# Kernel tuning notes

Measured on AMD Instinct MI355X. Metric: run time of the kernel, lower is better.

## Reference

```python
import jax, jax.numpy as jnp
import numpy as np

BINS = 64
LAMBDA_AFFINE = 1.0
LAMBDA_SIM = 1.0
EPS = 1e-10

B, C, D, H, W = 2, 1, 192, 224, 192


def setup_inputs() -> dict:
    key = jax.random.key(0)
    k1, k2, k3, k4 = jax.random.split(key, 4)
    return {
        "predicted_affine": jax.random.normal(k1, (B, 12), dtype=jnp.float32),
        "true_affine": jax.random.normal(k2, (B, 12), dtype=jnp.float32),
        "fixed": jax.random.uniform(k3, (B, C, D, H, W), dtype=jnp.float32),
        "warped": jax.random.uniform(k4, (B, C, D, H, W), dtype=jnp.float32),
    }


def _bin_indices(x_flat):
    # x_flat: (B, N) -> int32 bin indices in [0, BINS-1]
    xmin = x_flat.min(axis=1, keepdims=True)
    xmax = x_flat.max(axis=1, keepdims=True)
    norm = (x_flat - xmin) / (xmax - xmin + EPS) * (BINS - 1)
    return jnp.clip(norm.astype(jnp.int32), 0, BINS - 1)


def mutual_information(fixed, warped):
    # take first channel, flatten per sample
    f = fixed[:, 0].reshape(fixed.shape[0], -1)   # (B, N)
    w = warped[:, 0].reshape(warped.shape[0], -1)  # (B, N)
    b = f.shape[0]
    fi = _bin_indices(f)
    wi = _bin_indices(w)
    # joint histogram per batch via one fused scatter-add (segment_sum)
    batch_off = (jnp.arange(b, dtype=jnp.int32) * (BINS * BINS))[:, None]
    flat_idx = (batch_off + fi * BINS + wi).reshape(-1)
    counts = jax.ops.segment_sum(
        jnp.ones(flat_idx.shape, dtype=jnp.float32), flat_idx,
        num_segments=b * BINS * BINS)
    joint = counts.reshape(b, BINS, BINS)
    joint = joint / (joint.sum(axis=(1, 2), keepdims=True) + EPS)
    p_f = joint.sum(axis=2)  # (B, BINS)
    p_w = joint.sum(axis=1)  # (B, BINS)
    h_f = -jnp.sum(p_f * jnp.log(p_f + EPS), axis=1)
    h_w = -jnp.sum(p_w * jnp.log(p_w + EPS), axis=1)
    h_j = -jnp.sum(joint * jnp.log(joint + EPS), axis=(1, 2))
    mi = h_f + h_w - h_j
    nmi = 2.0 * mi / (h_f + h_w + EPS)  # normalized=True
    return -nmi.mean()


def reference(predicted_affine, true_affine, fixed, warped):
    affine_loss = jnp.mean((predicted_affine - true_affine) ** 2)
    similarity_loss = mutual_information(fixed, warped)
    total_loss = LAMBDA_AFFINE * affine_loss + LAMBDA_SIM * similarity_loss
    return total_loss
```

## Files before the change

kernel.cpp:

```cpp
#include <hip/hip_runtime.h>
#include <cfloat>
#include <math.h>

#define BINS 64
#define NELEM (192*224*192)
#define NB 2
#define HIST_OFF 16

__device__ __forceinline__ unsigned fkey(float f){
    unsigned u = __float_as_uint(f);
    return (u & 0x80000000u) ? ~u : (u | 0x80000000u);
}
__device__ __forceinline__ float funkey(unsigned k){
    unsigned u = (k & 0x80000000u) ? (k ^ 0x80000000u) : ~k;
    return __uint_as_float(u);
}

__global__ void k_init(unsigned* ws){
    int i = blockIdx.x * 256 + threadIdx.x;
    if (i < 16) ws[i] = ((i & 1) == 0) ? 0xFFFFFFFFu : 0u;
    if (i < NB * BINS * BINS) ws[HIST_OFF + i] = 0u;
}

__global__ void k_minmax(const float* __restrict__ F, const float* __restrict__ W,
                         unsigned* ws){
    const int b = blockIdx.y;
    const float4* F4 = (const float4*)(F + (size_t)b * NELEM);
    const float4* W4 = (const float4*)(W + (size_t)b * NELEM);
    const int n4 = NELEM / 4;
    float fmn = FLT_MAX, fmx = -FLT_MAX, wmn = FLT_MAX, wmx = -FLT_MAX;
    for (int i = blockIdx.x * blockDim.x + threadIdx.x; i < n4;
         i += gridDim.x * blockDim.x){
        float4 a = F4[i], c = W4[i];
        fmn = fminf(fmn, fminf(fminf(a.x, a.y), fminf(a.z, a.w)));
        fmx = fmaxf(fmx, fmaxf(fmaxf(a.x, a.y), fmaxf(a.z, a.w)));
        wmn = fminf(wmn, fminf(fminf(c.x, c.y), fminf(c.z, c.w)));
        wmx = fmaxf(wmx, fmaxf(fmaxf(c.x, c.y), fmaxf(c.z, c.w)));
    }
    for (int off = 32; off; off >>= 1){
        fmn = fminf(fmn, __shfl_down(fmn, off));
        fmx = fmaxf(fmx, __shfl_down(fmx, off));
        wmn = fminf(wmn, __shfl_down(wmn, off));
        wmx = fmaxf(wmx, __shfl_down(wmx, off));
    }
    __shared__ float s[4][4];
    int wave = threadIdx.x >> 6;
    if ((threadIdx.x & 63) == 0){
        s[wave][0] = fmn; s[wave][1] = fmx; s[wave][2] = wmn; s[wave][3] = wmx;
    }
    __syncthreads();
    if (threadIdx.x == 0){
        float a0 = s[0][0], a1 = s[0][1], a2 = s[0][2], a3 = s[0][3];
        for (int wv = 1; wv < 4; ++wv){
            a0 = fminf(a0, s[wv][0]); a1 = fmaxf(a1, s[wv][1]);
            a2 = fminf(a2, s[wv][2]); a3 = fmaxf(a3, s[wv][3]);
        }
        atomicMin(&ws[b*4+0], fkey(a0));
        atomicMax(&ws[b*4+1], fkey(a1));
        atomicMin(&ws[b*4+2], fkey(a2));
        atomicMax(&ws[b*4+3], fkey(a3));
    }
}

__global__ void k_hist(const float* __restrict__ F, const float* __restrict__ W,
                       unsigned* ws){
    const int b = blockIdx.y;
    __shared__ unsigned h[BINS * BINS];
    for (int i = threadIdx.x; i < BINS * BINS; i += blockDim.x) h[i] = 0u;
    __syncthreads();
    const float fmn = funkey(ws[b*4+0]);
    const float fmx = funkey(ws[b*4+1]);
    const float wmn = funkey(ws[b*4+2]);
    const float wmx = funkey(ws[b*4+3]);
    const float fden = fmx - fmn + 1e-10f;
    const float wden = wmx - wmn + 1e-10f;
    const float4* F4 = (const float4*)(F + (size_t)b * NELEM);
    const float4* W4 = (const float4*)(W + (size_t)b * NELEM);
    const int n4 = NELEM / 4;
    for (int i = blockIdx.x * blockDim.x + threadIdx.x; i < n4;
         i += gridDim.x * blockDim.x){
        float4 a = F4[i], c = W4[i];
        float fa[4] = {a.x, a.y, a.z, a.w};
        float wa[4] = {c.x, c.y, c.z, c.w};
        #pragma unroll
        for (int k = 0; k < 4; ++k){
            int fi = (int)((fa[k] - fmn) / fden * 63.0f);
            int wi = (int)((wa[k] - wmn) / wden * 63.0f);
            fi = min(max(fi, 0), 63);
            wi = min(max(wi, 0), 63);
            atomicAdd(&h[fi * BINS + wi], 1u);
        }
    }
    __syncthreads();
    unsigned* gh = ws + HIST_OFF + b * BINS * BINS;
    for (int i = threadIdx.x; i < BINS * BINS; i += blockDim.x){
        unsigned v = h[i];
        if (v) atomicAdd(&gh[i], v);
    }
}

__device__ double block_sum256(double v, double* sred){
    int t = threadIdx.x;
    sred[t] = v; __syncthreads();
    for (int off = 128; off; off >>= 1){
        if (t < off) sred[t] += sred[t + off];
        __syncthreads();
    }
    double r = sred[0]; __syncthreads();
    return r;
}

__global__ void k_final(const float* __restrict__ pa, const float* __restrict__ ta,
                        const unsigned* __restrict__ ws, float* __restrict__ out){
    __shared__ double sred[256];
    const unsigned* hist = ws + HIST_OFF;
    const double invN = 1.0 / (double)NELEM;
    double loss_sim = 0.0;
    for (int b = 0; b < NB; ++b){
        const unsigned* H = hist + b * BINS * BINS;
        double hj_p = 0.0;
        for (int i = threadIdx.x; i < BINS * BINS; i += 256){
            double p = (double)H[i] * invN;
            hj_p += p * log(p + 1e-10);
        }
        double hj = -block_sum256(hj_p, sred);
        double hf_p = 0.0, hw_p = 0.0;
        if (threadIdx.x < BINS){
            int r = threadIdx.x;
            double pf = 0.0, pw = 0.0;
            for (int j = 0; j < BINS; ++j){
                pf += (double)H[r * BINS + j];
                pw += (double)H[j * BINS + r];
            }
            pf *= invN; pw *= invN;
            hf_p = pf * log(pf + 1e-10);
            hw_p = pw * log(pw + 1e-10);
        }
        double hf = -block_sum256(hf_p, sred);
        double hw = -block_sum256(hw_p, sred);
        double mi  = hf + hw - hj;
        double nmi = 2.0 * mi / (hf + hw + 1e-10);
        loss_sim += -nmi;
    }
    loss_sim /= (double)NB;
    if (threadIdx.x == 0){
        double a = 0.0;
        for (int i = 0; i < 24; ++i){
            double d = (double)pa[i] - (double)ta[i];
            a += d * d;
        }
        a /= 24.0;
        out[0] = (float)(a + loss_sim);
    }
}

extern "C" void kernel_launch(void* const* d_in, const int* in_sizes, int n_in,
                              void* d_out, int out_size, void* d_ws, size_t ws_size,
                              hipStream_t stream) {
    const float* pa = (const float*)d_in[0];
    const float* ta = (const float*)d_in[1];
    const float* F  = (const float*)d_in[2];
    const float* W  = (const float*)d_in[3];
    float* out = (float*)d_out;
    unsigned* ws = (unsigned*)d_ws;

    k_init<<<dim3(32 + 1), 256, 0, stream>>>(ws);
    k_minmax<<<dim3(512, NB), 256, 0, stream>>>(F, W, ws);
    k_hist<<<dim3(256, NB), 256, 0, stream>>>(F, W, ws);
    k_final<<<1, 256, 0, stream>>>(pa, ta, ws, out);
}
```

Measured before the change: 242.4 us.

## Use one-tile-per-block grids with batched loads for minmax and histogram kernels

Replaces the grid-stride loops in the minmax and histogram kernels with fixed grids where each block handles 8 float4 per thread, issued as batched loads before any compute. Minmax now splits F and W into separate grid rows. The histogram loads are issued before the shared-memory clear so their latency overlaps it. The final kernel switches from double to float log and normalisation. This raises the number of blocks and the number of global atomics from per-block merges, and slightly lowers the precision of the entropy terms.

After: 282.4 us. +16.5%, slower.

```diff
diff --git a/kernel.cpp b/kernel.cpp
--- a/kernel.cpp
+++ b/kernel.cpp
@@ -4,8 +4,13 @@
 
 #define BINS 64
 #define NELEM (192*224*192)
+#define N4    (NELEM/4)
 #define NB 2
 #define HIST_OFF 16
+#define T4 8
+#define BLK 256
+#define PER_BLOCK (T4*BLK)
+#define NBLK_SLICE (N4/PER_BLOCK)
 
 __device__ __forceinline__ unsigned fkey(float f){
     unsigned u = __float_as_uint(f);
@@ -22,70 +27,82 @@
     if (i < NB * BINS * BINS) ws[HIST_OFF + i] = 0u;
 }
 
-__global__ void k_minmax(const float* __restrict__ F, const float* __restrict__ W,
-                         unsigned* ws){
-    const int b = blockIdx.y;
-    const float4* F4 = (const float4*)(F + (size_t)b * NELEM);
-    const float4* W4 = (const float4*)(W + (size_t)b * NELEM);
-    const int n4 = NELEM / 4;
-    float fmn = FLT_MAX, fmx = -FLT_MAX, wmn = FLT_MAX, wmx = -FLT_MAX;
-    for (int i = blockIdx.x * blockDim.x + threadIdx.x; i < n4;
-         i += gridDim.x * blockDim.x){
-        float4 a = F4[i], c = W4[i];
-        fmn = fminf(fmn, fminf(fminf(a.x, a.y), fminf(a.z, a.w)));
-        fmx = fmaxf(fmx, fmaxf(fmaxf(a.x, a.y), fmaxf(a.z, a.w)));
-        wmn = fminf(wmn, fminf(fminf(c.x, c.y), fminf(c.z, c.w)));
-        wmx = fmaxf(wmx, fmaxf(fmaxf(c.x, c.y), fmaxf(c.z, c.w)));
+__global__ __launch_bounds__(BLK) void k_minmax(const float* __restrict__ F,
+                                                const float* __restrict__ W,
+                                                unsigned* ws){
+    const int y = blockIdx.y;
+    const int b = y & 1;
+    const float4* S4 = (const float4*)((y < 2 ? F : W) + (size_t)b * NELEM);
+    const int base = blockIdx.x * PER_BLOCK + threadIdx.x;
+
+    float4 v[T4];
+    #pragma unroll
+    for (int k = 0; k < T4; ++k) v[k] = S4[base + k * BLK];
+
+    float4 mn4 = v[0], mx4 = v[0];
+    #pragma unroll
+    for (int k = 1; k < T4; ++k){
+        mn4.x = fminf(mn4.x, v[k].x); mn4.y = fminf(mn4.y, v[k].y);
+        mn4.z = fminf(mn4.z, v[k].z); mn4.w = fminf(mn4.w, v[k].w);
+        mx4.x = fmaxf(mx4.x, v[k].x); mx4.y = fmaxf(mx4.y, v[k].y);
+        mx4.z = fmaxf(mx4.z, v[k].z); mx4.w = fmaxf(mx4.w, v[k].w);
     }
+    float mn = fminf(fminf(mn4.x, mn4.y), fminf(mn4.z, mn4.w));
+    float mx = fmaxf(fmaxf(mx4.x, mx4.y), fmaxf(mx4.z, mx4.w));
+
     for (int off = 32; off; off >>= 1){
-        fmn = fminf(fmn, __shfl_down(fmn, off));
-        fmx = fmaxf(fmx, __shfl_down(fmx, off));
-        wmn = fminf(wmn, __shfl_down(wmn, off));
-        wmx = fmaxf(wmx, __shfl_down(wmx, off));
+        mn = fminf(mn, __shfl_down(mn, off));
+        mx = fmaxf(mx, __shfl_down(mx, off));
     }
-    __shared__ float s[4][4];
+    __shared__ float s[4][2];
     int wave = threadIdx.x >> 6;
-    if ((threadIdx.x & 63) == 0){
-        s[wave][0] = fmn; s[wave][1] = fmx; s[wave][2] = wmn; s[wave][3] = wmx;
-    }
+    if ((threadIdx.x & 63) == 0){ s[wave][0] = mn; s[wave][1] = mx; }
     __syncthreads();
     if (threadIdx.x == 0){
-        float a0 = s[0][0], a1 = s[0][1], a2 = s[0][2], a3 = s[0][3];
+        float a0 = s[0][0], a1 = s[0][1];
         for (int wv = 1; wv < 4; ++wv){
             a0 = fminf(a0, s[wv][0]); a1 = fmaxf(a1, s[wv][1]);
-            a2 = fminf(a2, s[wv][2]); a3 = fmaxf(a3, s[wv][3]);
         }
-        atomicMin(&ws[b*4+0], fkey(a0));
-        atomicMax(&ws[b*4+1], fkey(a1));
-        atomicMin(&ws[b*4+2], fkey(a2));
-        atomicMax(&ws[b*4+3], fkey(a3));
+        const int slot = b * 4 + (y < 2 ? 0 : 2);
+        atomicMin(&ws[slot],     fkey(a0));
+        atomicMax(&ws[slot + 1], fkey(a1));
     }
 }
 
-__global__ void k_hist(const float* __restrict__ F, const float* __restrict__ W,
-                       unsigned* ws){
+__global__ __launch_bounds__(BLK) void k_hist(const float* __restrict__ F,
+                                              const float* __restrict__ W,
+                                              unsigned* ws){
     const int b = blockIdx.y;
     __shared__ unsigned h[BINS * BINS];
-    for (int i = threadIdx.x; i < BINS * BINS; i += blockDim.x) h[i] = 0u;
-    __syncthreads();
+
     const float fmn = funkey(ws[b*4+0]);
     const float fmx = funkey(ws[b*4+1]);
     const float wmn = funkey(ws[b*4+2]);
     const float wmx = funkey(ws[b*4+3]);
     const float fden = fmx - fmn + 1e-10f;
     const float wden = wmx - wmn + 1e-10f;
+
     const float4* F4 = (const float4*)(F + (size_t)b * NELEM);
     const float4* W4 = (const float4*)(W + (size_t)b * NELEM);
-    const int n4 = NELEM / 4;
-    for (int i = blockIdx.x * blockDim.x + threadIdx.x; i < n4;
-         i += gridDim.x * blockDim.x){
-        float4 a = F4[i], c = W4[i];
-        float fa[4] = {a.x, a.y, a.z, a.w};
-        float wa[4] = {c.x, c.y, c.z, c.w};
+    const int base = blockIdx.x * PER_BLOCK + threadIdx.x;
+
+    float4 fv[T4], wv[T4];
+    #pragma unroll
+    for (int k = 0; k < T4; ++k) fv[k] = F4[base + k * BLK];
+    #pragma unroll
+    for (int k = 0; k < T4; ++k) wv[k] = W4[base + k * BLK];
+
+    for (int i = threadIdx.x; i < BINS * BINS; i += BLK) h[i] = 0u;
+    __syncthreads();
+
+    #pragma unroll
+    for (int k = 0; k < T4; ++k){
+        float fa[4] = {fv[k].x, fv[k].y, fv[k].z, fv[k].w};
+        float wa[4] = {wv[k].x, wv[k].y, wv[k].z, wv[k].w};
         #pragma unroll
-        for (int k = 0; k < 4; ++k){
-            int fi = (int)((fa[k] - fmn) / fden * 63.0f);
-            int wi = (int)((wa[k] - wmn) / wden * 63.0f);
+        for (int j = 0; j < 4; ++j){
+            int fi = (int)((fa[j] - fmn) / fden * 63.0f);
+            int wi = (int)((wa[j] - wmn) / wden * 63.0f);
             fi = min(max(fi, 0), 63);
             wi = min(max(wi, 0), 63);
             atomicAdd(&h[fi * BINS + wi], 1u);
@@ -93,7 +110,7 @@
     }
     __syncthreads();
     unsigned* gh = ws + HIST_OFF + b * BINS * BINS;
-    for (int i = threadIdx.x; i < BINS * BINS; i += blockDim.x){
+    for (int i = threadIdx.x; i < BINS * BINS; i += BLK){
         unsigned v = h[i];
         if (v) atomicAdd(&gh[i], v);
     }
@@ -114,27 +131,27 @@
                         const unsigned* __restrict__ ws, float* __restrict__ out){
     __shared__ double sred[256];
     const unsigned* hist = ws + HIST_OFF;
-    const double invN = 1.0 / (double)NELEM;
+    const float fN = (float)NELEM;
     double loss_sim = 0.0;
     for (int b = 0; b < NB; ++b){
         const unsigned* H = hist + b * BINS * BINS;
         double hj_p = 0.0;
         for (int i = threadIdx.x; i < BINS * BINS; i += 256){
-            double p = (double)H[i] * invN;
-            hj_p += p * log(p + 1e-10);
+            float p = (float)H[i] / fN;
+            hj_p += (double)(p * logf(p + 1e-10f));
         }
         double hj = -block_sum256(hj_p, sred);
         double hf_p = 0.0, hw_p = 0.0;
         if (threadIdx.x < BINS){
             int r = threadIdx.x;
-            double pf = 0.0, pw = 0.0;
+            unsigned cf = 0, cw = 0;
             for (int j = 0; j < BINS; ++j){
-                pf += (double)H[r * BINS + j];
-                pw += (double)H[j * BINS + r];
+                cf += H[r * BINS + j];
+                cw += H[j * BINS + r];
             }
-            pf *= invN; pw *= invN;
-            hf_p = pf * log(pf + 1e-10);
-            hw_p = pw * log(pw + 1e-10);
+            float pf = (float)cf / fN, pw = (float)cw / fN;
+            hf_p = (double)(pf * logf(pf + 1e-10f));
+            hw_p = (double)(pw * logf(pw + 1e-10f));
         }
         double hf = -block_sum256(hf_p, sred);
         double hw = -block_sum256(hw_p, sred);
@@ -164,8 +181,8 @@
     float* out = (float*)d_out;
     unsigned* ws = (unsigned*)d_ws;
 
-    k_init<<<dim3(32 + 1), 256, 0, stream>>>(ws);
-    k_minmax<<<dim3(512, NB), 256, 0, stream>>>(F, W, ws);
-    k_hist<<<dim3(256, NB), 256, 0, stream>>>(F, W, ws);
+    k_init<<<33, 256, 0, stream>>>(ws);
+    k_minmax<<<dim3(NBLK_SLICE, 4), BLK, 0, stream>>>(F, W, ws);
+    k_hist<<<dim3(NBLK_SLICE, NB), BLK, 0, stream>>>(F, W, ws);
     k_final<<<1, 256, 0, stream>>>(pa, ta, ws, out);
 }
```
